# Optimization experiments

Measured on AMD Instinct MI355X. Metric: run time of the kernel, lower is better.

Reference implementation:

```python
import jax, jax.numpy as jnp
import numpy as np

N = 100000   # nodes
E = 1600000  # edges per relation (avg in-degree 16)
D = 128      # gcn_hidden (in_feat == out_feat)
R = 2        # relations: forward_edge, backward_edge


def setup_inputs() -> dict:
    key = jax.random.key(0)
    ks = jax.random.split(key, 8)
    x = jax.random.normal(ks[0], (N, D), dtype=jnp.float32)
    src_fwd = jax.random.randint(ks[1], (E,), 0, N, dtype=jnp.int32)
    dst_fwd = jax.random.randint(ks[2], (E,), 0, N, dtype=jnp.int32)
    src_bwd = jax.random.randint(ks[3], (E,), 0, N, dtype=jnp.int32)
    dst_bwd = jax.random.randint(ks[4], (E,), 0, N, dtype=jnp.int32)
    # xavier_uniform with relu gain sqrt(2)
    gain = np.sqrt(2.0)
    lim_rel = gain * np.sqrt(6.0 / (D + D))
    rel_weight = jax.random.uniform(ks[5], (R, D, D), minval=-lim_rel, maxval=lim_rel, dtype=jnp.float32)
    loop_weight = jax.random.uniform(ks[6], (D, D), minval=-lim_rel, maxval=lim_rel, dtype=jnp.float32)
    h_bias = jnp.zeros((D,), dtype=jnp.float32)
    return {
        'x': x,
        'src_fwd': src_fwd, 'dst_fwd': dst_fwd,
        'src_bwd': src_bwd, 'dst_bwd': dst_bwd,
        'rel_weight': rel_weight, 'loop_weight': loop_weight, 'h_bias': h_bias,
    }


def _rel_conv(x, src, dst, W):
    # dgl GraphConv(norm='right', weight per relation): scatter-sum src feats to
    # dst, divide by clamped in-degree, then matmul W (in_feat == out_feat so
    # order of matmul vs aggregation is mathematically equivalent).
    msg = x[src]                                            # [E, D] gather
    agg = jax.ops.segment_sum(msg, dst, num_segments=N)     # [N, D] scatter-add
    deg = jax.ops.segment_sum(jnp.ones((src.shape[0],), x.dtype), dst, num_segments=N)
    agg = agg / jnp.clip(deg, 1.0)[:, None]                 # right norm, deg clamp(min=1)
    return agg @ W                                          # [N, D]


def reference(x, src_fwd, dst_fwd, src_bwd, dst_bwd, rel_weight, loop_weight, h_bias):
    h = _rel_conv(x, src_fwd, dst_fwd, rel_weight[0])
    h = h + _rel_conv(x, src_bwd, dst_bwd, rel_weight[1])   # HeteroGraphConv sums per-relation results
    h = h + x @ loop_weight                                 # self loop
    h = h + h_bias                                          # bias
    h = jax.nn.relu(h)                                      # activation
    return h                                                # dropout is identity in eval
```

## Files before the change

kernel.cpp:

```cpp
#include <hip/hip_runtime.h>
#include <hip/hip_bf16.h>


#define DFEAT 128
#define CH2 4096
#define PSH 6
#define NBMAX 3200
#define CAPB 1536
#define NPACK 24

typedef __attribute__((ext_vector_type(8))) short short8v;
typedef __attribute__((ext_vector_type(4))) float float4v;
typedef __attribute__((ext_vector_type(2))) unsigned int u2v;
typedef __attribute__((ext_vector_type(4))) unsigned short ushort4v;

__global__ __launch_bounds__(256) void front_kernel(
        const float4v* __restrict__ x4, ushort4v* __restrict__ xb4, int n4,
        const int* __restrict__ src0, const int* __restrict__ dst0,
        const int* __restrict__ src1, const int* __restrict__ dst1,
        int* __restrict__ cursor, unsigned* __restrict__ binned,
        const float* __restrict__ wrel, const float* __restrict__ wloop,
        unsigned short* __restrict__ wb,
        int Np, int E, int nbin) {
    __shared__ unsigned cntp[NBMAX / 2];
    __shared__ int base[NBMAX];
    int tid = threadIdx.x;
    int bid = blockIdx.x;

    if (bid < nbin) {
        auto ldp = [&](int i) {
            int r = (i >= E) ? 1 : 0;
            int e = i - r * E;
            int t = r ? dst1[e] : dst0[e];
            return r * Np + t;
        };
        auto lds_ = [&](int i) {
            int r = (i >= E) ? 1 : 0;
            int e = i - r * E;
            return r ? src1[e] : src0[e];
        };
        for (int i = tid; i < NBMAX / 2; i += 256) cntp[i] = 0;
        __syncthreads();
        int lo = bid * CH2, hi = min(2 * E, lo + CH2);
        for (int ii = lo + tid; ii < hi; ii += 1024) {
            int p0 = ldp(ii);
            int p1 = (ii + 256 < hi) ? ldp(ii + 256) : -1;
            int p2 = (ii + 512 < hi) ? ldp(ii + 512) : -1;
            int p3 = (ii + 768 < hi) ? ldp(ii + 768) : -1;
            int b0 = p0 >> PSH;
            atomicAdd(&cntp[b0 >> 1], (b0 & 1) ? 0x10000u : 1u);
            if (p1 >= 0) { int b1 = p1 >> PSH; atomicAdd(&cntp[b1 >> 1], (b1 & 1) ? 0x10000u : 1u); }
            if (p2 >= 0) { int b2 = p2 >> PSH; atomicAdd(&cntp[b2 >> 1], (b2 & 1) ? 0x10000u : 1u); }
            if (p3 >= 0) { int b3 = p3 >> PSH; atomicAdd(&cntp[b3 >> 1], (b3 & 1) ? 0x10000u : 1u); }
        }
        __syncthreads();
        for (int b = tid; b < NBMAX; b += 256) {
            int c = (int)((cntp[b >> 1] >> ((b & 1) * 16)) & 0xFFFFu);
            if (c) base[b] = b * CAPB + atomicAdd(&cursor[b], c);
        }
        __syncthreads();
        for (int ii = lo + tid; ii < hi; ii += 1024) {
            int p0 = ldp(ii);             int s0 = lds_(ii);
            int i1 = ii + 256, i2 = ii + 512, i3 = ii + 768;
            int p1 = (i1 < hi) ? ldp(i1) : -1;  int s1 = (i1 < hi) ? lds_(i1) : 0;
            int p2 = (i2 < hi) ? ldp(i2) : -1;  int s2 = (i2 < hi) ? lds_(i2) : 0;
            int p3 = (i3 < hi) ? ldp(i3) : -1;  int s3 = (i3 < hi) ? lds_(i3) : 0;
            { int slot = atomicAdd(&base[p0 >> PSH], 1);
              binned[slot] = ((unsigned)(p0 & 63) << 17) | (unsigned)s0; }
            if (p1 >= 0) { int slot = atomicAdd(&base[p1 >> PSH], 1);
                           binned[slot] = ((unsigned)(p1 & 63) << 17) | (unsigned)s1; }
            if (p2 >= 0) { int slot = atomicAdd(&base[p2 >> PSH], 1);
                           binned[slot] = ((unsigned)(p2 & 63) << 17) | (unsigned)s2; }
            if (p3 >= 0) { int slot = atomicAdd(&base[p3 >> PSH], 1);
                           binned[slot] = ((unsigned)(p3 & 63) << 17) | (unsigned)s3; }
        }
    } else if (bid < nbin + NPACK) {
        int t = (bid - nbin) * 256 + tid;
        if (t < 12 * 8 * 64) {
            int lane = t & 63;
            int kbase = (t >> 9) * 32 + (lane >> 4) * 8;
            int col = (((t >> 6) & 7) << 4) + (lane & 15);
            unsigned short tmp[8];
#pragma unroll
            for (int j = 0; j < 8; ++j) {
                int k = kbase + j;
                float v = (k < 256) ? wrel[k * DFEAT + col]
                                    : wloop[(k - 256) * DFEAT + col];
                tmp[j] = __hip_bfloat16_raw(__float2bfloat16(v)).x;
            }
            *(ushort4*)(wb + t * 8)     = make_ushort4(tmp[0], tmp[1], tmp[2], tmp[3]);
            *(ushort4*)(wb + t * 8 + 4) = make_ushort4(tmp[4], tmp[5], tmp[6], tmp[7]);
        }
    } else {
        int cb = bid - nbin - NPACK;
#pragma unroll
        for (int k = 0; k < 4; ++k) {
            int i = cb * 1024 + k * 256 + tid;
            if (i < n4) {
                float4v v = __builtin_nontemporal_load(x4 + i);
                ushort4v o;
                o[0] = __hip_bfloat16_raw(__float2bfloat16(v[0])).x;
                o[1] = __hip_bfloat16_raw(__float2bfloat16(v[1])).x;
                o[2] = __hip_bfloat16_raw(__float2bfloat16(v[2])).x;
                o[3] = __hip_bfloat16_raw(__float2bfloat16(v[3])).x;
                xb4[i] = o;
            }
        }
    }
}

#define CONSUME(Q0, Q1, Q2, Q3) {                                              \
    a[0] += __uint_as_float(Q0[0] << 16) + __uint_as_float(Q1[0] << 16)        \
          + __uint_as_float(Q2[0] << 16) + __uint_as_float(Q3[0] << 16);       \
    a[1] += __uint_as_float(Q0[0] & 0xffff0000u) + __uint_as_float(Q1[0] & 0xffff0000u) \
          + __uint_as_float(Q2[0] & 0xffff0000u) + __uint_as_float(Q3[0] & 0xffff0000u); \
    a[2] += __uint_as_float(Q0[1] << 16) + __uint_as_float(Q1[1] << 16)        \
          + __uint_as_float(Q2[1] << 16) + __uint_as_float(Q3[1] << 16);       \
    a[3] += __uint_as_float(Q0[1] & 0xffff0000u) + __uint_as_float(Q1[1] & 0xffff0000u) \
          + __uint_as_float(Q2[1] & 0xffff0000u) + __uint_as_float(Q3[1] & 0xffff0000u); }

__global__ __launch_bounds__(256) void aggmm_kernel(
        const u2v* __restrict__ xb2,
        const unsigned short* __restrict__ xb,
        const unsigned* __restrict__ binned,
        const int* __restrict__ cursor,
        const unsigned short* __restrict__ wb,
        const float* __restrict__ bias,
        float* __restrict__ out, int N, int NBH) {
    __shared__ unsigned ebuf[CAPB];
    __shared__ __align__(16) unsigned short Atile[64][136];
    __shared__ int cnt[64], cur[64], rs[64];
    int tid = threadIdx.x;
    int g = blockIdx.x;
    int hw = tid >> 5, lane = tid & 31;
    int wv = tid >> 6, l64 = tid & 63;
    int mrow = l64 & 15, quad = l64 >> 4;

    float4v acc[8];
#pragma unroll
    for (int ct = 0; ct < 8; ++ct) acc[ct] = (float4v){0.f, 0.f, 0.f, 0.f};

    for (int rel = 0; rel < 2; ++rel) {
        int b = rel ? (NBH + g) : g;
        int total = min(cursor[b], CAPB);
        const unsigned* seg = binned + (size_t)b * CAPB;

        if (tid < 64) cnt[tid] = 0;
        __syncthreads();
        for (int i = tid; i < total; i += 256)
            atomicAdd(&cnt[seg[i] >> 17], 1);
        __syncthreads();
        if (tid < 64) {
            int c = cnt[tid];
            int inc = c;
#pragma unroll
            for (int off = 1; off < 64; off <<= 1) {
                int t2 = __shfl_up(inc, off);
                if (tid >= off) inc += t2;
            }
            rs[tid] = inc - c;
            cur[tid] = inc - c;
        }
        __syncthreads();
        for (int i = tid; i < total; i += 256) {
            unsigned v = seg[i];
            int slot = atomicAdd(&cur[v >> 17], 1);
            ebuf[slot] = v & 0x1FFFFu;
        }
        __syncthreads();

        for (int pi = 0; pi < 8; ++pi) {
            int pl = hw * 8 + pi;
            int s0 = rs[pl], c = cnt[pl];
            float4v a = (float4v){0.f, 0.f, 0.f, 0.f};
            int e = 0;
            if (c >= 8) {
                u2v A0 = xb2[(size_t)ebuf[s0]     * 32 + lane];
                u2v B0 = xb2[(size_t)ebuf[s0 + 1] * 32 + lane];
                u2v C0 = xb2[(size_t)ebuf[s0 + 2] * 32 + lane];
                u2v D0 = xb2[(size_t)ebuf[s0 + 3] * 32 + lane];
                u2v A1 = xb2[(size_t)ebuf[s0 + 4] * 32 + lane];
                u2v B1 = xb2[(size_t)ebuf[s0 + 5] * 32 + lane];
                u2v C1 = xb2[(size_t)ebuf[s0 + 6] * 32 + lane];
                u2v D1 = xb2[(size_t)ebuf[s0 + 7] * 32 + lane];
                for (e = 8; e + 4 <= c; e += 4) {
                    u2v nA = xb2[(size_t)ebuf[s0 + e]     * 32 + lane];
                    u2v nB = xb2[(size_t)ebuf[s0 + e + 1] * 32 + lane];
                    u2v nC = xb2[(size_t)ebuf[s0 + e + 2] * 32 + lane];
                    u2v nD = xb2[(size_t)ebuf[s0 + e + 3] * 32 + lane];
                    CONSUME(A0, B0, C0, D0);
                    A0 = A1; B0 = B1; C0 = C1; D0 = D1;
                    A1 = nA; B1 = nB; C1 = nC; D1 = nD;
                }
                CONSUME(A0, B0, C0, D0);
                CONSUME(A1, B1, C1, D1);
            } else if (c >= 4) {
                u2v A0 = xb2[(size_t)ebuf[s0]     * 32 + lane];
                u2v B0 = xb2[(size_t)ebuf[s0 + 1] * 32 + lane];
                u2v C0 = xb2[(size_t)ebuf[s0 + 2] * 32 + lane];
                u2v D0 = xb2[(size_t)ebuf[s0 + 3] * 32 + lane];
                CONSUME(A0, B0, C0, D0);
                e = 4;
            }
            for (; e < c; ++e) {
                int s = ebuf[s0 + e];
                u2v gq = xb2[(size_t)s * 32 + lane];
                a[0] += __uint_as_float(gq[0] << 16);
                a[1] += __uint_as_float(gq[0] & 0xffff0000u);
                a[2] += __uint_as_float(gq[1] << 16);
                a[3] += __uint_as_float(gq[1] & 0xffff0000u);
            }
            float inv = 1.0f / (float)max(c, 1);
            ushort4v w;
            w[0] = __hip_bfloat16_raw(__float2bfloat16(a[0] * inv)).x;
            w[1] = __hip_bfloat16_raw(__float2bfloat16(a[1] * inv)).x;
            w[2] = __hip_bfloat16_raw(__float2bfloat16(a[2] * inv)).x;
            w[3] = __hip_bfloat16_raw(__float2bfloat16(a[3] * inv)).x;
            *(ushort4v*)&Atile[pl][4 * lane] = w;
        }
        __syncthreads();

#pragma unroll
        for (int kc4 = 0; kc4 < 4; ++kc4) {
            int kc = rel * 4 + kc4;
            short8v a0 = *(const short8v*)&Atile[wv * 16 + mrow][kc4 * 32 + quad * 8];
#pragma unroll
            for (int ct = 0; ct < 8; ++ct) {
                short8v bfr = *(const short8v*)(wb + (((kc * 8 + ct) << 6) + l64) * 8);
                acc[ct] = __builtin_amdgcn_mfma_f32_16x16x32_bf16(a0, bfr, acc[ct], 0, 0, 0);
            }
        }
        __syncthreads();
    }

    int n0 = min(g * 64 + wv * 16 + mrow, N - 1);
#pragma unroll
    for (int kc = 8; kc < 12; ++kc) {
        short8v a0 = *(const short8v*)(xb + (size_t)n0 * DFEAT + (kc & 3) * 32 + quad * 8);
#pragma unroll
        for (int ct = 0; ct < 8; ++ct) {
            short8v bfr = *(const short8v*)(wb + (((kc * 8 + ct) << 6) + l64) * 8);
            acc[ct] = __builtin_amdgcn_mfma_f32_16x16x32_bf16(a0, bfr, acc[ct], 0, 0, 0);
        }
    }

#pragma unroll
    for (int ct = 0; ct < 8; ++ct) {
        int col = ct * 16 + mrow;
        float bv = bias[col];
#pragma unroll
        for (int i = 0; i < 4; ++i) {
            int row = g * 64 + wv * 16 + quad * 4 + i;
            if (row < N)
                __builtin_nontemporal_store(fmaxf(acc[ct][i] + bv, 0.f),
                                            out + (size_t)row * DFEAT + col);
        }
    }
}

extern "C" void kernel_launch(void* const* d_in, const int* in_sizes, int n_in,
                              void* d_out, int out_size, void* d_ws, size_t ws_size,
                              hipStream_t stream) {
    const float* x      = (const float*)d_in[0];
    const int* src_fwd  = (const int*)d_in[1];
    const int* dst_fwd  = (const int*)d_in[2];
    const int* src_bwd  = (const int*)d_in[3];
    const int* dst_bwd  = (const int*)d_in[4];
    const float* wrel   = (const float*)d_in[5];
    const float* wloop  = (const float*)d_in[6];
    const float* hbias  = (const float*)d_in[7];
    float* out          = (float*)d_out;

    int N = in_sizes[0] / DFEAT;
    int E = in_sizes[1];
    int TE = 2 * E;
    int Npad = (N + 63) & ~63;
    int NBH = Npad >> 6;
    int NB = 2 * NBH;

    unsigned short* wb   = (unsigned short*)d_ws;
    unsigned* binned     = (unsigned*)(wb + 12 * 8 * 64 * 8);
    unsigned short* xb   = (unsigned short*)(binned + (size_t)NB * CAPB);
    int* cursor          = (int*)(xb + (size_t)(N + 1) * DFEAT);

    int n4 = N * (DFEAT / 4);
    int nconv = (n4 + 1023) / 1024;
    int nbin = (TE + CH2 - 1) / CH2;

    (void)hipMemsetAsync(cursor, 0, NB * sizeof(int), stream);

    front_kernel<<<nbin + NPACK + nconv, 256, 0, stream>>>(
        (const float4v*)x, (ushort4v*)xb, n4,
        src_fwd, dst_fwd, src_bwd, dst_bwd,
        cursor, binned, wrel, wloop, wb, Npad, E, nbin);

    aggmm_kernel<<<NBH, 256, 0, stream>>>(
        (const u2v*)xb, xb, binned, cursor, wb, hbias, out, N, NBH);
}
```

Before: 357.7 us.

## Split bin cursors into sub-buckets and halve aggregation block to 32 rows

The binning pass now spreads atomic cursor updates over 8 sub-cursors per bin (chosen by block id), each owning a 192-slot region of the bin, to cut contention on the global cursor atomics. The aggregation kernel launches twice as many 128-thread blocks, each handling 32 of the 64 rows in a bin. Each block scans all 1536 slots of the bin and keeps only its half, so segment reads are duplicated. Sub-bucket capacity is smaller, raising the risk of overflow truncation on skewed bins.

```diff
diff --git a/kernel.cpp b/kernel.cpp
--- a/kernel.cpp
+++ b/kernel.cpp
@@ -6,7 +6,10 @@
 #define CH2 4096
 #define PSH 6
 #define NBMAX 3200
+#define KSUB 8
+#define CAPS 192
 #define CAPB 1536
+#define EBUFN 1024
 #define NPACK 24
 
 typedef __attribute__((ext_vector_type(8))) short short8v;
@@ -21,7 +24,7 @@
         int* __restrict__ cursor, unsigned* __restrict__ binned,
         const float* __restrict__ wrel, const float* __restrict__ wloop,
         unsigned short* __restrict__ wb,
-        int Np, int E, int nbin) {
+        int Np, int E, int NB, int nbin) {
     __shared__ unsigned cntp[NBMAX / 2];
     __shared__ int base[NBMAX];
     int tid = threadIdx.x;
@@ -39,6 +42,7 @@
             int e = i - r * E;
             return r ? src1[e] : src0[e];
         };
+        int k = bid & (KSUB - 1);
         for (int i = tid; i < NBMAX / 2; i += 256) cntp[i] = 0;
         __syncthreads();
         int lo = bid * CH2, hi = min(2 * E, lo + CH2);
@@ -56,7 +60,7 @@
         __syncthreads();
         for (int b = tid; b < NBMAX; b += 256) {
             int c = (int)((cntp[b >> 1] >> ((b & 1) * 16)) & 0xFFFFu);
-            if (c) base[b] = b * CAPB + atomicAdd(&cursor[b], c);
+            if (c) base[b] = b * CAPB + k * CAPS + atomicAdd(&cursor[k * NB + b], c);
         }
         __syncthreads();
         for (int ii = lo + tid; ii < hi; ii += 1024) {
@@ -83,9 +87,9 @@
             unsigned short tmp[8];
 #pragma unroll
             for (int j = 0; j < 8; ++j) {
-                int k = kbase + j;
-                float v = (k < 256) ? wrel[k * DFEAT + col]
-                                    : wloop[(k - 256) * DFEAT + col];
+                int kk = kbase + j;
+                float v = (kk < 256) ? wrel[kk * DFEAT + col]
+                                     : wloop[(kk - 256) * DFEAT + col];
                 tmp[j] = __hip_bfloat16_raw(__float2bfloat16(v)).x;
             }
             *(ushort4*)(wb + t * 8)     = make_ushort4(tmp[0], tmp[1], tmp[2], tmp[3]);
@@ -94,8 +98,8 @@
     } else {
         int cb = bid - nbin - NPACK;
 #pragma unroll
-        for (int k = 0; k < 4; ++k) {
-            int i = cb * 1024 + k * 256 + tid;
+        for (int kk = 0; kk < 4; ++kk) {
+            int i = cb * 1024 + kk * 256 + tid;
             if (i < n4) {
                 float4v v = __builtin_nontemporal_load(x4 + i);
                 ushort4v o;
@@ -119,19 +123,21 @@
     a[3] += __uint_as_float(Q0[1] & 0xffff0000u) + __uint_as_float(Q1[1] & 0xffff0000u) \
           + __uint_as_float(Q2[1] & 0xffff0000u) + __uint_as_float(Q3[1] & 0xffff0000u); }
 
-__global__ __launch_bounds__(256) void aggmm_kernel(
+__global__ __launch_bounds__(128) void aggmm_kernel(
         const u2v* __restrict__ xb2,
         const unsigned short* __restrict__ xb,
         const unsigned* __restrict__ binned,
         const int* __restrict__ cursor,
         const unsigned short* __restrict__ wb,
         const float* __restrict__ bias,
-        float* __restrict__ out, int N, int NBH) {
-    __shared__ unsigned ebuf[CAPB];
-    __shared__ __align__(16) unsigned short Atile[64][136];
-    __shared__ int cnt[64], cur[64], rs[64];
+        float* __restrict__ out, int N, int NB, int NBH) {
+    __shared__ unsigned ebuf[EBUFN];
+    __shared__ __align__(16) unsigned short Atile[32][136];
+    __shared__ int cnt[32], cur[32], rs[32];
+    __shared__ int scnt[KSUB];
     int tid = threadIdx.x;
     int g = blockIdx.x;
+    int bb = g >> 1, hf = g & 1;
     int hw = tid >> 5, lane = tid & 31;
     int wv = tid >> 6, l64 = tid & 63;
     int mrow = l64 & 15, quad = l64 >> 4;
@@ -141,20 +147,26 @@
     for (int ct = 0; ct < 8; ++ct) acc[ct] = (float4v){0.f, 0.f, 0.f, 0.f};
 
     for (int rel = 0; rel < 2; ++rel) {
-        int b = rel ? (NBH + g) : g;
-        int total = min(cursor[b], CAPB);
+        int b = rel * NBH + bb;
         const unsigned* seg = binned + (size_t)b * CAPB;
 
-        if (tid < 64) cnt[tid] = 0;
-        __syncthreads();
-        for (int i = tid; i < total; i += 256)
-            atomicAdd(&cnt[seg[i] >> 17], 1);
-        __syncthreads();
-        if (tid < 64) {
+        if (tid < 32) cnt[tid] = 0;
+        if (tid < KSUB) scnt[tid] = min(cursor[tid * NB + b], CAPS);
+        __syncthreads();
+        for (int i = tid; i < CAPB; i += 128) {
+            int k = (i * 683) >> 17;
+            if (i - k * CAPS < scnt[k]) {
+                unsigned v = seg[i];
+                int p6 = (int)(v >> 17) & 63;
+                if ((p6 >> 5) == hf) atomicAdd(&cnt[p6 & 31], 1);
+            }
+        }
+        __syncthreads();
+        if (tid < 32) {
             int c = cnt[tid];
             int inc = c;
 #pragma unroll
-            for (int off = 1; off < 64; off <<= 1) {
+            for (int off = 1; off < 32; off <<= 1) {
                 int t2 = __shfl_up(inc, off);
                 if (tid >= off) inc += t2;
             }
@@ -162,16 +174,24 @@
             cur[tid] = inc - c;
         }
         __syncthreads();
-        for (int i = tid; i < total; i += 256) {
-            unsigned v = seg[i];
-            int slot = atomicAdd(&cur[v >> 17], 1);
-            ebuf[slot] = v & 0x1FFFFu;
+        for (int i = tid; i < CAPB; i += 128) {
+            int k = (i * 683) >> 17;
+            if (i - k * CAPS < scnt[k]) {
+                unsigned v = seg[i];
+                int p6 = (int)(v >> 17) & 63;
+                if ((p6 >> 5) == hf) {
+                    int slot = atomicAdd(&cur[p6 & 31], 1);
+                    if (slot < EBUFN) ebuf[slot] = v & 0x1FFFFu;
+                }
+            }
         }
         __syncthreads();
 
         for (int pi = 0; pi < 8; ++pi) {
             int pl = hw * 8 + pi;
-            int s0 = rs[pl], c = cnt[pl];
+            int s0 = rs[pl];
+            int c = cnt[pl];
+            if (s0 >= EBUFN) c = 0; else c = min(c, EBUFN - s0);
             float4v a = (float4v){0.f, 0.f, 0.f, 0.f};
             int e = 0;
             if (c >= 8) {
@@ -233,7 +253,7 @@
         __syncthreads();
     }
 
-    int n0 = min(g * 64 + wv * 16 + mrow, N - 1);
+    int n0 = min(g * 32 + wv * 16 + mrow, N - 1);
 #pragma unroll
     for (int kc = 8; kc < 12; ++kc) {
         short8v a0 = *(const short8v*)(xb + (size_t)n0 * DFEAT + (kc & 3) * 32 + quad * 8);
@@ -250,7 +270,7 @@
         float bv = bias[col];
 #pragma unroll
         for (int i = 0; i < 4; ++i) {
-            int row = g * 64 + wv * 16 + quad * 4 + i;
+            int row = g * 32 + wv * 16 + quad * 4 + i;
             if (row < N)
                 __builtin_nontemporal_store(fmaxf(acc[ct][i] + bv, 0.f),
                                             out + (size_t)row * DFEAT + col);
@@ -287,13 +307,13 @@
     int nconv = (n4 + 1023) / 1024;
     int nbin = (TE + CH2 - 1) / CH2;
 
-    (void)hipMemsetAsync(cursor, 0, NB * sizeof(int), stream);
+    (void)hipMemsetAsync(cursor, 0, KSUB * NB * sizeof(int), stream);
 
     front_kernel<<<nbin + NPACK + nconv, 256, 0, stream>>>(
         (const float4v*)x, (ushort4v*)xb, n4,
         src_fwd, dst_fwd, src_bwd, dst_bwd,
-        cursor, binned, wrel, wloop, wb, Npad, E, nbin);
-
-    aggmm_kernel<<<NBH, 256, 0, stream>>>(
-        (const u2v*)xb, xb, binned, cursor, wb, hbias, out, N, NBH);
+        cursor, binned, wrel, wloop, wb, Npad, E, NB, nbin);
+
+    aggmm_kernel<<<2 * NBH, 128, 0, stream>>>(
+        (const u2v*)xb, xb, binned, cursor, wb, hbias, out, N, NB, NBH);
 }
```

Result: faster. 346.8 us (-3.0%).
